# Optimization experiments

Measured on AMD Instinct MI355X. Metric: run time of the kernel, lower is better.

Reference implementation:

```python
import jax, jax.numpy as jnp
import numpy as np
import math

K = 8       # wavelet order (k)
C = 8       # channels (c)
ALPHA = 64  # retained Fourier modes
L = 0       # coarsest level
B = 32
N = 8192    # power of two


def setup_inputs() -> dict:
    key = jax.random.key(0)
    ks = jax.random.split(key, 14)
    ck = C * K
    scale = 1.0 / (ck * ck)  # matches torch: 1/(c*k)**2
    f32 = jnp.float32
    inp = {
        "x": jax.random.normal(ks[0], (B, N, C, K), dtype=f32),
        # SparseKernelFT1d weights (complex, stored as re/im): scale * rand
        "wA_re": scale * jax.random.uniform(ks[1], (ck, ck, ALPHA), dtype=f32),
        "wA_im": scale * jax.random.uniform(ks[2], (ck, ck, ALPHA), dtype=f32),
        "wB_re": scale * jax.random.uniform(ks[3], (ck, ck, ALPHA), dtype=f32),
        "wB_im": scale * jax.random.uniform(ks[4], (ck, ck, ALPHA), dtype=f32),
        "wC_re": scale * jax.random.uniform(ks[5], (ck, ck, ALPHA), dtype=f32),
        "wC_im": scale * jax.random.uniform(ks[6], (ck, ck, ALPHA), dtype=f32),
        # T0 linear layer (k -> k)
        "T0_w": jax.random.normal(ks[7], (K, K), dtype=f32) / math.sqrt(K),
        "T0_b": 0.01 * jax.random.normal(ks[8], (K,), dtype=f32),
        # Legendre wavelet filter buffers: ec_* are [H0.T;H1.T] / [G0.T;G1.T] (2k,k),
        # rc_* are [H0;G0] / [H1;G1] (2k,k). Stand-ins: random orthonormal-ish matrices
        # scaled like wavelet filters (same math regardless of exact values).
        "ec_s": jax.random.normal(ks[9], (2 * K, K), dtype=f32) / math.sqrt(2 * K),
        "ec_d": jax.random.normal(ks[10], (2 * K, K), dtype=f32) / math.sqrt(2 * K),
        "rc_e": jax.random.normal(ks[11], (2 * K, K), dtype=f32) / math.sqrt(2 * K),
        "rc_o": jax.random.normal(ks[12], (2 * K, K), dtype=f32) / math.sqrt(2 * K),
    }
    return inp


def _sparse_ft(x, w_re, w_im):
    # x: [B, N, c, k] -> spectral mixing over first ALPHA rfft modes
    Bb, Nn, c, k = x.shape
    xv = x.reshape(Bb, Nn, c * k).transpose(0, 2, 1)   # [B, ck, N]
    xf = jnp.fft.rfft(xv)                               # [B, ck, N//2+1] complex
    l = min(ALPHA, Nn // 2 + 1)
    W = (w_re[:, :, :l] + 1j * w_im[:, :, :l]).astype(jnp.complex64)
    of = jnp.einsum('bix,iox->box', xf[:, :, :l], W)
    out_ft = jnp.zeros((Bb, c * k, Nn // 2 + 1), dtype=jnp.complex64).at[:, :, :l].set(of)
    xo = jnp.fft.irfft(out_ft, n=Nn)                    # [B, ck, N] real
    return xo.transpose(0, 2, 1).reshape(Bb, Nn, c, k)


def reference(x, wA_re, wA_im, wB_re, wB_im, wC_re, wC_im, T0_w, T0_b,
              ec_s, ec_d, rc_e, rc_o):
    Bb, Nn, c, k = x.shape
    ns = int(math.floor(math.log2(Nn)))
    Ud, Us = [], []
    # --- decomposition ---
    for _ in range(ns - L):
        xa = jnp.concatenate([x[:, ::2], x[:, 1::2]], axis=-1)  # [B, N/2, c, 2k]
        d = xa @ ec_d                                           # [B, N/2, c, k]
        s = xa @ ec_s
        Ud.append(_sparse_ft(d, wA_re, wA_im) + _sparse_ft(s, wB_re, wB_im))
        Us.append(_sparse_ft(d, wC_re, wC_im))
        x = s
    # --- coarsest-level linear ---
    x = x @ T0_w.T + T0_b
    # --- reconstruction (u_s is None branch) ---
    for i in range(ns - 1 - L, -1, -1):
        x = x + Us[i]
        xc = jnp.concatenate([x, Ud[i]], axis=-1)               # [B, n, c, 2k]
        x_e = xc @ rc_e
        x_o = xc @ rc_o
        Bc, Nc, cc, _ = xc.shape
        x = jnp.stack([x_e, x_o], axis=2).reshape(Bc, Nc * 2, cc, K)  # interleave even/odd
    return (x,) + tuple(Ud) + tuple(Us)
```

## Files before the change

kernel.cpp:

```cpp
#include <hip/hip_runtime.h>

#define BB 32
#define CKD 64
#define CC 8
#define KK 8
#define FPW 132

__device__ const int D_FCB[14] = {0,32,48,56,60,62,63,64,65,66,67,68,69,70};
__device__ const int D_TB[14] = {0,64,96,112,120,124,126,127,128,129,130,131,132,133};
__device__ const int D_L[13]  = {64,64,64,64,64,64,33,17,9,5,3,2,1};
__device__ const int D_FTOF[13] = {0,524288,786432,917504,983040,1015808,1032192,
                                   1048576,1064960,1081344,1097728,1114112,1130496};
__device__ const int D_XP[65] = {0,13,25,36,46,56,65,74,83,92,100,108,116,124,132,140,
    148,156,163,170,177,184,191,198,205,212,219,226,233,240,247,254,261,268,274,280,
    286,292,298,304,310,316,322,328,334,340,346,352,358,364,370,376,382,388,394,400,
    406,412,418,424,430,436,442,448,454};

typedef __attribute__((ext_vector_type(4))) short s4v;
typedef __attribute__((ext_vector_type(8))) short s8v;
typedef __attribute__((ext_vector_type(4))) float f4v;

static __device__ __forceinline__ float4 ld4(const float* p){ return *(const float4*)p; }
static __device__ __forceinline__ size_t d_udo(int i){ return 33554432ull - (16777216u >> i); }
static __device__ __forceinline__ size_t d_uso(int i){ return 50329600ull - (16777216u >> i); }
static __device__ __forceinline__ size_t d_tof(int i){ return 128ull * (8192u - (8192u >> i)); }

static __device__ __forceinline__ unsigned short b16(float f) {
    unsigned u = __float_as_uint(f);
    u += 0x7FFFu + ((u >> 16) & 1u);
    return (unsigned short)(u >> 16);
}
static __device__ __forceinline__ float fb16(unsigned short h) {
    return __uint_as_float(((unsigned)h) << 16);
}

__global__ __launch_bounds__(256) void gen_tbl2_k(unsigned short* __restrict__ Th,
        unsigned short* __restrict__ Tl, unsigned short* __restrict__ Tfh,
        unsigned short* __restrict__ Tfl) {
    int lvl = blockIdx.y;
    int nh = 4096 >> lvl;
    int idx = blockIdx.x * 256 + threadIdx.x;
    if (blockIdx.z == 0) {
        if (idx >= nh * 128) return;
        int t = idx >> 7, k = idx & 127, x = k >> 1;
        int l = nh / 2 + 1; if (l > 64) l = 64;
        float v = 0.f;
        if (x < l) {
            int r = (x * t) & (nh - 1);
            float th = 6.283185307179586f * ((float)r / (float)nh);
            float s, c; sincosf(th, &s, &c);
            v = (k & 1) ? s : c;
        }
        unsigned short hi = b16(v);
        unsigned short lo = b16(v - fb16(hi));
        size_t off = d_tof(lvl) + idx;
        Th[off] = hi; Tl[off] = lo;
    } else {
        int nhp = nh < 128 ? 128 : nh;
        if (idx >= 128 * nhp) return;
        int j = idx & 7;
        int lane = (idx >> 3) & 63;
        int mt = (idx >> 9) & 7;
        int kb = idx >> 12;
        int row = mt*16 + (lane & 15);
        int t = kb*32 + (lane >> 4)*8 + j;
        int x = row >> 1;
        int l = nh / 2 + 1; if (l > 64) l = 64;
        float v = 0.f;
        if (x < l && t < nh) {
            int r = (x * t) & (nh - 1);
            float th = 6.283185307179586f * ((float)r / (float)nh);
            float s, c; sincosf(th, &s, &c);
            v = (row & 1) ? -s : c;
        }
        unsigned short hi = b16(v);
        unsigned short lo = b16(v - fb16(hi));
        size_t off = (size_t)D_FTOF[lvl] + idx;
        Tfh[off] = hi; Tfl[off] = lo;
    }
}

__global__ __launch_bounds__(256) void wtr_k(const float* __restrict__ wAr,
        const float* __restrict__ wAi, const float* __restrict__ wBr,
        const float* __restrict__ wBi, const float* __restrict__ wCr,
        const float* __restrict__ wCi, float* __restrict__ wt) {
    int x = blockIdx.x, arr = blockIdx.y;
    const float* W;
    switch (arr) {
        case 0: W = wAr; break;
        case 1: W = wAi; break;
        case 2: W = wBr; break;
        case 3: W = wBi; break;
        case 4: W = wCr; break;
        default: W = wCi; break;
    }
    float* o = wt + ((size_t)arr*64 + x)*4096;
    for (int q = threadIdx.x; q < 4096; q += 256)
        o[q] = W[(size_t)q*64 + x];
}

__global__ __launch_bounds__(256) void wbig_k(const float* __restrict__ wt,
        unsigned short* __restrict__ wbh, unsigned short* __restrict__ wbl) {
    int x = blockIdx.x;
    int f0 = blockIdx.y * 2048;
    for (int q = threadIdx.x; q < 2048; q += 256) {
        int f = f0 + q;
        int j = f & 7;
        int lane = (f >> 3) & 63;
        int nt = (f >> 9) & 15;
        int kt = f >> 13;
        int k = kt*32 + (lane >> 4)*8 + j;
        int n = nt*16 + (lane & 15);
        int pk = k >> 6, i = k & 63;
        int pn = n >> 6, o = n & 63;
        int arr; float sgn;
        switch ((pn << 2) | pk) {
            case 0:  arr = 0; sgn =  1.f; break;
            case 1:  arr = 1; sgn = -1.f; break;
            case 2:  arr = 2; sgn =  1.f; break;
            case 3:  arr = 3; sgn = -1.f; break;
            case 4:  arr = 1; sgn = -1.f; break;
            case 5:  arr = 0; sgn = -1.f; break;
            case 6:  arr = 3; sgn = -1.f; break;
            case 7:  arr = 2; sgn = -1.f; break;
            case 8:  arr = 4; sgn =  1.f; break;
            case 9:  arr = 5; sgn = -1.f; break;
            case 12: arr = 5; sgn = -1.f; break;
            case 13: arr = 4; sgn = -1.f; break;
            default: arr = -1; sgn = 0.f; break;
        }
        float v = 0.f;
        if (arr >= 0) v = sgn * wt[((size_t)arr*64 + x)*4096 + (size_t)i*64 + o];
        unsigned short h = b16(v);
        unsigned short l2 = b16(v - fb16(h));
        wbh[(size_t)x*65536 + f] = h;
        wbl[(size_t)x*65536 + f] = l2;
    }
}

__global__ __launch_bounds__(256) void decomp_k(const float* __restrict__ xin,
        const float* __restrict__ ecd, const float* __restrict__ ecs,
        float* __restrict__ dslot, float* __restrict__ sslot, int nh) {
    int idx = blockIdx.x * 256 + threadIdx.x;
    if (idx >= BB * nh * CC) return;
    int c = idx & 7;
    int t = (idx >> 3) % nh;
    int b = idx / (nh * CC);
    const float* p0 = xin + ((size_t)b * 2 * nh + 2 * t) * CKD + c * KK;
    float xa[16];
    float4 v;
    v = ld4(p0);      xa[0]=v.x; xa[1]=v.y; xa[2]=v.z; xa[3]=v.w;
    v = ld4(p0+4);    xa[4]=v.x; xa[5]=v.y; xa[6]=v.z; xa[7]=v.w;
    v = ld4(p0+64);   xa[8]=v.x; xa[9]=v.y; xa[10]=v.z; xa[11]=v.w;
    v = ld4(p0+68);   xa[12]=v.x; xa[13]=v.y; xa[14]=v.z; xa[15]=v.w;
    float dd[8], ss[8];
    #pragma unroll
    for (int m = 0; m < 8; m++) { dd[m] = 0.f; ss[m] = 0.f; }
    #pragma unroll
    for (int j = 0; j < 16; j++) {
        float xv = xa[j];
        #pragma unroll
        for (int m = 0; m < 8; m++) {
            dd[m] = fmaf(xv, ecd[j*8+m], dd[m]);
            ss[m] = fmaf(xv, ecs[j*8+m], ss[m]);
        }
    }
    size_t ob = ((size_t)b * nh + t) * CKD + c * KK;
    *(float4*)(dslot+ob)   = make_float4(dd[0],dd[1],dd[2],dd[3]);
    *(float4*)(dslot+ob+4) = make_float4(dd[4],dd[5],dd[6],dd[7]);
    *(float4*)(sslot+ob)   = make_float4(ss[0],ss[1],ss[2],ss[3]);
    *(float4*)(sslot+ob+4) = make_float4(ss[4],ss[5],ss[6],ss[7]);
}

__global__ __launch_bounds__(256) void decomp_small_k(const float* __restrict__ s4base,
        const float* __restrict__ ecd, const float* __restrict__ ecs,
        const float* __restrict__ T0w, const float* __restrict__ T0b,
        float* __restrict__ outbuf, float* __restrict__ xt0) {
    __shared__ float sA[128*64];
    __shared__ float sB[64*64];
    int b = blockIdx.x, tid = threadIdx.x;
    for (int lvl = 5; lvl <= 12; lvl++) {
        int nh = 4096 >> lvl;
        const float* src = (lvl == 5) ? (s4base + (size_t)b*256*CKD)
                                      : (((lvl - 6) & 1) ? sB : sA);
        float* dst = ((lvl - 5) & 1) ? sB : sA;
        float* dG = outbuf + d_udo(lvl) + (size_t)b*nh*CKD;
        float* sG = outbuf + d_uso(lvl) + (size_t)b*nh*CKD;
        for (int q = tid; q < nh*8; q += 256) {
            int c = q & 7, t = q >> 3;
            const float* p0 = src + (size_t)(2*t)*CKD + c*KK;
            float xa[16];
            float4 v;
            v = ld4(p0);      xa[0]=v.x; xa[1]=v.y; xa[2]=v.z; xa[3]=v.w;
            v = ld4(p0+4);    xa[4]=v.x; xa[5]=v.y; xa[6]=v.z; xa[7]=v.w;
            v = ld4(p0+64);   xa[8]=v.x; xa[9]=v.y; xa[10]=v.z; xa[11]=v.w;
            v = ld4(p0+68);   xa[12]=v.x; xa[13]=v.y; xa[14]=v.z; xa[15]=v.w;
            float dd[8], ss[8];
            #pragma unroll
            for (int m = 0; m < 8; m++) { dd[m] = 0.f; ss[m] = 0.f; }
            #pragma unroll
            for (int j = 0; j < 16; j++) {
                float xv = xa[j];
                #pragma unroll
                for (int m = 0; m < 8; m++) {
                    dd[m] = fmaf(xv, ecd[j*8+m], dd[m]);
                    ss[m] = fmaf(xv, ecs[j*8+m], ss[m]);
                }
            }
            size_t ob = (size_t)t * CKD + c * KK;
            *(float4*)(dG+ob)   = make_float4(dd[0],dd[1],dd[2],dd[3]);
            *(float4*)(dG+ob+4) = make_float4(dd[4],dd[5],dd[6],dd[7]);
            *(float4*)(sG+ob)   = make_float4(ss[0],ss[1],ss[2],ss[3]);
            *(float4*)(sG+ob+4) = make_float4(ss[4],ss[5],ss[6],ss[7]);
            float* dl = dst + t*CKD + c*KK;
            #pragma unroll
            for (int j = 0; j < 8; j++) dl[j] = ss[j];
        }
        __syncthreads();
    }
    if (tid < 64) {
        int m = tid & 7, c = tid >> 3;
        const float* xr = sB + c*KK;
        float a = T0b[m];
        #pragma unroll
        for (int j = 0; j < 8; j++) a = fmaf(xr[j], T0w[m*8+j], a);
        xt0[(size_t)b*64 + tid] = a;
    }
}

__global__ __launch_bounds__(256) void fft_fwd_mfma_k(const float* __restrict__ outbuf,
        const unsigned short* __restrict__ Tfh, const unsigned short* __restrict__ Tfl,
        float* __restrict__ xfpf, float2* __restrict__ xf_all) {
    __shared__ unsigned vp[128*FPW];
    int slot = blockIdx.x;
    int lvl = 0;
    while (lvl < 12 && slot >= D_FCB[lvl+1]) lvl++;
    int nh = 4096 >> lvl;
    int ch = D_FCB[lvl+1] - D_FCB[lvl];
    int t0s = (slot - D_FCB[lvl]) * 128;
    int b = blockIdx.y;
    const float* V0 = outbuf + d_udo(lvl) + (size_t)b * nh * CKD;
    const float* V1 = outbuf + d_uso(lvl) + (size_t)b * nh * CKD;
    const unsigned short* THb = Tfh + D_FTOF[lvl];
    const unsigned short* TLb = Tfl + D_FTOF[lvl];
    int tid = threadIdx.x;
    int w = tid >> 6, lane = tid & 63;
    int col = lane & 15, khi = lane >> 4;
    int mt0 = w * 2;
    #pragma unroll
    for (int q = 0; q < 16; q++) {
        int fi = tid + 256*q;
        int tl_ = fi >> 5;
        int t = t0s + tl_;
        int iq = fi & 31;
        int z = iq >> 4;
        int i4 = (iq & 15) * 4;
        const float* Vz = z ? V1 : V0;
        float4 v = make_float4(0.f,0.f,0.f,0.f);
        if (t < nh) v = ld4(Vz + (size_t)t*CKD + i4);
        const float* pv = &v.x;
        int rowb = z*64 + i4;
        #pragma unroll
        for (int j = 0; j < 4; j++) {
            int row = rowb + j;
            float f = pv[j];
            unsigned u = __float_as_uint(f);
            unsigned hi = u & 0xFFFF0000u;
            float r = f - __uint_as_float(hi);
            unsigned lo = __float_as_uint(r) & 0xFFFF0000u;
            int cw = tl_ ^ (((row >> 3) & 7) << 2);
            vp[row*FPW + cw] = (hi >> 16) | lo;
        }
    }
    __syncthreads();
    int rrow[8], rswz[8];
    #pragma unroll
    for (int n = 0; n < 8; n++) {
        rrow[n] = n*16 + col;
        rswz[n] = ((rrow[n] >> 3) & 7) << 2;
    }
    f4v acc[2][8];
    #pragma unroll
    for (int m = 0; m < 2; m++)
        #pragma unroll
        for (int n = 0; n < 8; n++) acc[m][n] = (f4v){0.f,0.f,0.f,0.f};
    int kb0 = (slot - D_FCB[lvl]) * 4;
    #pragma unroll
    for (int kk = 0; kk < 4; kk++) {
        int kb = kb0 + kk;
        s8v ah[2], al[2];
        #pragma unroll
        for (int m = 0; m < 2; m++) {
            size_t fo = (((size_t)kb*8 + (mt0 + m))*64 + lane)*8;
            ah[m] = *(const s8v*)(THb + fo);
            al[m] = *(const s8v*)(TLb + fo);
        }
        int cb = kk*32 + khi*8;
        #pragma unroll
        for (int n = 0; n < 8; n++) {
            const unsigned* pr = vp + rrow[n]*FPW;
            uint4 w0 = *(const uint4*)(pr + (cb ^ rswz[n]));
            uint4 w1 = *(const uint4*)(pr + ((cb + 4) ^ rswz[n]));
            s8v bh, bl;
            const unsigned* pw = &w0.x;
            #pragma unroll
            for (int j = 0; j < 4; j++) {
                bh[j] = (short)(pw[j] & 0xFFFFu);
                bl[j] = (short)(pw[j] >> 16);
            }
            pw = &w1.x;
            #pragma unroll
            for (int j = 0; j < 4; j++) {
                bh[4+j] = (short)(pw[j] & 0xFFFFu);
                bl[4+j] = (short)(pw[j] >> 16);
            }
            #pragma unroll
            for (int m = 0; m < 2; m++) {
                acc[m][n] = __builtin_amdgcn_mfma_f32_16x16x32_bf16(ah[m], bh, acc[m][n], 0,0,0);
                acc[m][n] = __builtin_amdgcn_mfma_f32_16x16x32_bf16(ah[m], bl, acc[m][n], 0,0,0);
                acc[m][n] = __builtin_amdgcn_mfma_f32_16x16x32_bf16(al[m], bh, acc[m][n], 0,0,0);
            }
        }
    }
    if (ch == 1) {
        float* XB = (float*)xf_all + (size_t)lvl*524288 + (size_t)b*16384;
        #pragma unroll
        for (int m = 0; m < 2; m++) {
            int m0 = (mt0 + m)*16 + khi*4;
            #pragma unroll
            for (int n = 0; n < 8; n++) {
                int ic = n*16 + col;
                int z = ic >> 6, i = ic & 63;
                float* X = XB + (size_t)z*8192;
                #pragma unroll
                for (int r = 0; r < 4; r++) {
                    int row = m0 + r;
                    X[(((size_t)(row >> 1)*64 + i) << 1) | (row & 1)] = acc[m][n][r];
                }
            }
        }
    } else {
        #pragma unroll
        for (int m = 0; m < 2; m++) {
            int m0 = (mt0 + m)*16 + khi*4;
            #pragma unroll
            for (int n = 0; n < 8; n++) {
                int ic = n*16 + col;
                int z = ic >> 6, i = ic & 63;
                float* P = xfpf + ((size_t)slot*64 + (size_t)b*2 + z) * 8192;
                #pragma unroll
                for (int r = 0; r < 4; r++)
                    P[(size_t)(m0 + r)*64 + i] = acc[m][n][r];
            }
        }
    }
}

__global__ __launch_bounds__(256) void reduce_fwd_k(const float* __restrict__ xfpf,
        float2* __restrict__ xf_all) {
    int lvl = blockIdx.y;
    int e = blockIdx.x * 256 + threadIdx.x;
    int j = e & 4095;
    int bz = e >> 12;
    int x = j >> 6, i = j & 63;
    int c0 = D_FCB[lvl], c1 = D_FCB[lvl+1];
    float re = 0.f, im = 0.f;
    for (int c = c0; c < c1; c++) {
        size_t base = ((size_t)c*64 + bz) * 8192;
        re += xfpf[base + (size_t)(2*x)*64 + i];
        im += xfpf[base + (size_t)(2*x+1)*64 + i];
    }
    xf_all[(size_t)lvl*262144 + (size_t)bz*4096 + j] = make_float2(re, im);
}

__global__ __launch_bounds__(256) void mix_mfma_k(const float2* __restrict__ xf_all,
        const unsigned short* __restrict__ wbh, const unsigned short* __restrict__ wbl,
        unsigned short* __restrict__ ofh, unsigned short* __restrict__ ofl) {
    __shared__ unsigned ax[32*260];
    int x = 0;
    while (x < 64 && (int)blockIdx.x >= D_XP[x+1]) x++;
    int lvl = blockIdx.x - D_XP[x];
    int nh = 4096 >> lvl;
    const float2* xfL = xf_all + (size_t)lvl*262144;
    int tid = threadIdx.x;
    for (int q = tid; q < 4096; q += 256) {
        int b = q >> 7, z = (q >> 6) & 1, i = q & 63;
        float2 v = xfL[((size_t)b*2 + z)*4096 + (size_t)x*64 + i];
        int sw = ((b >> 3) & 7) << 2;
        int kR = z*128 + i;
        unsigned uR = __float_as_uint(v.x);
        unsigned hiR = uR & 0xFFFF0000u;
        float rR = v.x - __uint_as_float(hiR);
        unsigned loR = __float_as_uint(rR) & 0xFFFF0000u;
        ax[b*260 + (kR ^ sw)] = (hiR >> 16) | loR;
        unsigned uI = __float_as_uint(v.y);
        unsigned hiI = uI & 0xFFFF0000u;
        float rI = v.y - __uint_as_float(hiI);
        unsigned loI = __float_as_uint(rI) & 0xFFFF0000u;
        ax[b*260 + ((kR + 64) ^ sw)] = (hiI >> 16) | loI;
    }
    __syncthreads();
    int w4 = tid >> 6, lane = tid & 63;
    int col = lane & 15, khi = lane >> 4;
    int mt = w4 & 1, nt0 = (w4 >> 1) * 8;
    int arow = mt*16 + col;
    int asw = ((arow >> 3) & 7) << 2;
    const unsigned* ap = ax + arow*260;
    const unsigned short* WBH = wbh + (size_t)x*65536;
    const unsigned short* WBL = wbl + (size_t)x*65536;
    f4v acc[8];
    #pragma unroll
    for (int n = 0; n < 8; n++) acc[n] = (f4v){0.f,0.f,0.f,0.f};
    #pragma unroll
    for (int kt = 0; kt < 8; kt++) {
        int cb = kt*32 + khi*8;
        uint4 a0 = *(const uint4*)(ap + (cb ^ asw));
        uint4 a1 = *(const uint4*)(ap + ((cb + 4) ^ asw));
        s8v ah, al;
        const unsigned* pw = &a0.x;
        #pragma unroll
        for (int j = 0; j < 4; j++) {
            ah[j] = (short)(pw[j] & 0xFFFFu);
            al[j] = (short)(pw[j] >> 16);
        }
        pw = &a1.x;
        #pragma unroll
        for (int j = 0; j < 4; j++) {
            ah[4+j] = (short)(pw[j] & 0xFFFFu);
            al[4+j] = (short)(pw[j] >> 16);
        }
        #pragma unroll
        for (int n = 0; n < 8; n++) {
            int nt = nt0 + n;
            size_t fo = (((size_t)kt*16 + nt)*64 + lane)*8;
            s8v bh = *(const s8v*)(WBH + fo);
            s8v bl = *(const s8v*)(WBL + fo);
            acc[n] = __builtin_amdgcn_mfma_f32_16x16x32_bf16(ah, bh, acc[n], 0, 0, 0);
            acc[n] = __builtin_amdgcn_mfma_f32_16x16x32_bf16(ah, bl, acc[n], 0, 0, 0);
            acc[n] = __builtin_amdgcn_mfma_f32_16x16x32_bf16(al, bh, acc[n], 0, 0, 0);
        }
    }
    float wfac = (x == 0 || 2*x == nh) ? 1.f : 2.f;
    float sc = wfac / (float)nh;
    int k0 = 2*x;
    #pragma unroll
    for (int n = 0; n < 8; n++) {
        int nn = nt0 + n;
        int pn = nn >> 2;
        int o = (nn & 3)*16 + col;
        int z = pn >> 1;
        int kr = k0 + (pn & 1);
        #pragma unroll
        for (int r = 0; r < 4; r++) {
            int b = mt*16 + khi*4 + r;
            size_t base = (((size_t)lvl*32 + b)*2 + z)*8192 + (size_t)kr*64 + o;
            float v = sc * acc[n][r];
            unsigned short h = b16(v);
            unsigned short l2 = b16(v - fb16(h));
            ofh[base] = h;
            ofl[base] = l2;
        }
    }
}

__global__ __launch_bounds__(256) void fft_inv_mfma_k(
        const unsigned short* __restrict__ ofh, const unsigned short* __restrict__ ofl,
        const unsigned short* __restrict__ Th,  const unsigned short* __restrict__ Tl,
        float* __restrict__ outbuf) {
    __shared__ unsigned short gh[2*64*132];
    __shared__ unsigned short gl[2*64*132];
    int lvl = 0;
    while (lvl < 12 && (int)blockIdx.x >= D_TB[lvl+1]) lvl++;
    int g = blockIdx.x - D_TB[lvl];
    int nh = 4096 >> lvl;
    int tbase = g * 64;
    int b = blockIdx.y;
    int tid = threadIdx.x;
    #pragma unroll
    for (int q = 0; q < 8; q++) {
        int fi = tid + 256*q;
        int z = fi >> 10;
        int r = fi & 1023;
        int k = r & 127, oct = r >> 7;
        const unsigned short* Gh = ofh + (((size_t)lvl*32 + b)*2 + z)*8192;
        const unsigned short* Gl = ofl + (((size_t)lvl*32 + b)*2 + z)*8192;
        uint4 vh = *(const uint4*)(Gh + (size_t)k*64 + oct*8);
        uint4 vl = *(const uint4*)(Gl + (size_t)k*64 + oct*8);
        const unsigned* ph = &vh.x;
        const unsigned* pl = &vl.x;
        #pragma unroll
        for (int i = 0; i < 8; i++) {
            unsigned wd = ph[i>>1];
            gh[z*8448 + (oct*8+i)*132 + k] = (i&1) ? (unsigned short)(wd>>16) : (unsigned short)(wd&0xFFFF);
            wd = pl[i>>1];
            gl[z*8448 + (oct*8+i)*132 + k] = (i&1) ? (unsigned short)(wd>>16) : (unsigned short)(wd&0xFFFF);
        }
    }
    __syncthreads();
    int w = tid >> 6;
    int lane = tid & 63;
    int tb = tbase + w*16;
    if (tb >= nh) return;
    int trow = lane & 15, khi = lane >> 4;
    int tA = tb + trow; if (tA >= nh) tA = nh - 1;
    const unsigned short* THp = Th + d_tof(lvl) + (size_t)tA*128 + khi*8;
    const unsigned short* TLp = Tl + d_tof(lvl) + (size_t)tA*128 + khi*8;
    f4v acc[8];
    #pragma unroll
    for (int n = 0; n < 8; n++) acc[n] = (f4v){0.f,0.f,0.f,0.f};
    #pragma unroll
    for (int kk = 0; kk < 4; kk++) {
        s8v ah = *(const s8v*)(THp + kk*32);
        s8v al = *(const s8v*)(TLp + kk*32);
        #pragma unroll
        for (int n = 0; n < 8; n++) {
            int z = n >> 2;
            int off = z*8448 + ((n & 3)*16 + trow)*132 + kk*32 + khi*8;
            s4v b0 = *(const s4v*)(gh + off);
            s4v b1 = *(const s4v*)(gh + off + 4);
            s4v c0 = *(const s4v*)(gl + off);
            s4v c1 = *(const s4v*)(gl + off + 4);
            s8v bh = __builtin_shufflevector(b0, b1, 0,1,2,3,4,5,6,7);
            s8v bl = __builtin_shufflevector(c0, c1, 0,1,2,3,4,5,6,7);
            acc[n] = __builtin_amdgcn_mfma_f32_16x16x32_bf16(ah, bh, acc[n], 0, 0, 0);
            acc[n] = __builtin_amdgcn_mfma_f32_16x16x32_bf16(ah, bl, acc[n], 0, 0, 0);
            acc[n] = __builtin_amdgcn_mfma_f32_16x16x32_bf16(al, bh, acc[n], 0, 0, 0);
        }
    }
    float* U0 = outbuf + d_udo(lvl) + (size_t)b * nh * CKD;
    float* U1 = outbuf + d_uso(lvl) + (size_t)b * nh * CKD;
    int thi4 = khi * 4;
    #pragma unroll
    for (int n = 0; n < 8; n++) {
        float* U = (n >> 2) ? U1 : U0;
        int ocol = (n & 3)*16 + trow;
        #pragma unroll
        for (int r = 0; r < 4; r++) {
            int t = tb + thi4 + r;
            if (t < nh) U[(size_t)t*64 + ocol] = acc[n][r];
        }
    }
}

__global__ __launch_bounds__(256) void recon_small_k(const float* __restrict__ xt0,
        const float* __restrict__ outbuf,
        const float* __restrict__ rce, const float* __restrict__ rco,
        float* __restrict__ rb0) {
    __shared__ float xA[128*64];
    __shared__ float xB[64*64];
    int b = blockIdx.x, tid = threadIdx.x;
    if (tid < 64) xB[tid] = xt0[(size_t)b*64 + tid];
    __syncthreads();
    for (int i = 12; i >= 6; i--) {
        int nh = 4096 >> i;
        const float* cur = ((i == 12) || !(i & 1)) ? xB : xA;
        float* nxt = (i & 1) ? xB : xA;
        const float* Us = outbuf + d_uso(i) + (size_t)b*nh*CKD;
        const float* Ud = outbuf + d_udo(i) + (size_t)b*nh*CKD;
        for (int q = tid; q < nh*8; q += 256) {
            int c = q & 7, t = q >> 3;
            size_t base = (size_t)t*CKD + c*KK;
            float xc[16];
            float4 a0 = ld4(cur+base), a1 = ld4(cur+base+4);
            float4 u0 = ld4(Us+base),  u1 = ld4(Us+base+4);
            float4 d0 = ld4(Ud+base),  d1 = ld4(Ud+base+4);
            xc[0]=a0.x+u0.x; xc[1]=a0.y+u0.y; xc[2]=a0.z+u0.z; xc[3]=a0.w+u0.w;
            xc[4]=a1.x+u1.x; xc[5]=a1.y+u1.y; xc[6]=a1.z+u1.z; xc[7]=a1.w+u1.w;
            xc[8]=d0.x;  xc[9]=d0.y;  xc[10]=d0.z; xc[11]=d0.w;
            xc[12]=d1.x; xc[13]=d1.y; xc[14]=d1.z; xc[15]=d1.w;
            float e[8], o2[8];
            #pragma unroll
            for (int m = 0; m < 8; m++) { e[m] = 0.f; o2[m] = 0.f; }
            #pragma unroll
            for (int j = 0; j < 16; j++) {
                float xv = xc[j];
                #pragma unroll
                for (int m = 0; m < 8; m++) {
                    e[m]  = fmaf(xv, rce[j*8+m], e[m]);
                    o2[m] = fmaf(xv, rco[j*8+m], o2[m]);
                }
            }
            if (i > 6) {
                float* pe = nxt + (size_t)(2*t)*CKD + c*KK;
                #pragma unroll
                for (int j = 0; j < 8; j++) { pe[j] = e[j]; pe[CKD + j] = o2[j]; }
            } else {
                float* pe = rb0 + ((size_t)b*128 + 2*t)*CKD + c*KK;
                *(float4*)(pe)      = make_float4(e[0],e[1],e[2],e[3]);
                *(float4*)(pe+4)    = make_float4(e[4],e[5],e[6],e[7]);
                *(float4*)(pe+64)   = make_float4(o2[0],o2[1],o2[2],o2[3]);
                *(float4*)(pe+68)   = make_float4(o2[4],o2[5],o2[6],o2[7]);
            }
        }
        __syncthreads();
    }
}

__global__ __launch_bounds__(256) void recon_k(const float* __restrict__ xin,
        const float* __restrict__ us, const float* __restrict__ ud,
        const float* __restrict__ rce, const float* __restrict__ rco,
        float* __restrict__ xout, int nh) {
    int idx = blockIdx.x*256 + threadIdx.x;
    if (idx >= BB*nh*CC) return;
    int c = idx & 7;
    int t = (idx >> 3) % nh;
    int b = idx / (nh*CC);
    size_t base = ((size_t)b*nh + t)*CKD + c*KK;
    float xc[16];
    float4 a0 = ld4(xin+base), a1 = ld4(xin+base+4);
    float4 u0 = ld4(us+base),  u1 = ld4(us+base+4);
    float4 d0 = ld4(ud+base),  d1 = ld4(ud+base+4);
    xc[0]=a0.x+u0.x; xc[1]=a0.y+u0.y; xc[2]=a0.z+u0.z; xc[3]=a0.w+u0.w;
    xc[4]=a1.x+u1.x; xc[5]=a1.y+u1.y; xc[6]=a1.z+u1.z; xc[7]=a1.w+u1.w;
    xc[8]=d0.x;  xc[9]=d0.y;  xc[10]=d0.z; xc[11]=d0.w;
    xc[12]=d1.x; xc[13]=d1.y; xc[14]=d1.z; xc[15]=d1.w;
    float e[8], o2[8];
    #pragma unroll
    for (int m = 0; m < 8; m++) { e[m] = 0.f; o2[m] = 0.f; }
    #pragma unroll
    for (int j = 0; j < 16; j++) {
        float xv = xc[j];
        #pragma unroll
        for (int m = 0; m < 8; m++) {
            e[m]  = fmaf(xv, rce[j*8+m], e[m]);
            o2[m] = fmaf(xv, rco[j*8+m], o2[m]);
        }
    }
    size_t ob = ((size_t)b*2*nh + 2*t)*CKD + c*KK;
    *(float4*)(xout+ob)      = make_float4(e[0],e[1],e[2],e[3]);
    *(float4*)(xout+ob+4)    = make_float4(e[4],e[5],e[6],e[7]);
    *(float4*)(xout+ob+64)   = make_float4(o2[0],o2[1],o2[2],o2[3]);
    *(float4*)(xout+ob+68)   = make_float4(o2[4],o2[5],o2[6],o2[7]);
}

extern "C" void kernel_launch(void* const* d_in, const int* in_sizes, int n_in,
                              void* d_out, int out_size, void* d_ws, size_t ws_size,
                              hipStream_t stream) {
    const float* x   = (const float*)d_in[0];
    const float* wAr = (const float*)d_in[1];
    const float* wAi = (const float*)d_in[2];
    const float* wBr = (const float*)d_in[3];
    const float* wBi = (const float*)d_in[4];
    const float* wCr = (const float*)d_in[5];
    const float* wCi = (const float*)d_in[6];
    const float* T0w = (const float*)d_in[7];
    const float* T0b = (const float*)d_in[8];
    const float* ecs = (const float*)d_in[9];
    const float* ecd = (const float*)d_in[10];
    const float* rce = (const float*)d_in[11];
    const float* rco = (const float*)d_in[12];
    float* out = (float*)d_out;
    float* wsf = (float*)d_ws;

    size_t p = 0;
    float2* xf_all = (float2*)(wsf + p); p += 6815744;
    unsigned short* ofh = (unsigned short*)(wsf + p); p += 3407872;
    unsigned short* ofl = (unsigned short*)(wsf + p); p += 3407872;
    unsigned short* Th  = (unsigned short*)(wsf + p); p += 528384;
    unsigned short* Tl  = (unsigned short*)(wsf + p); p += 528384;
    unsigned short* Tfh = (unsigned short*)(wsf + p); p += 573440;
    unsigned short* Tfl = (unsigned short*)(wsf + p); p += 573440;
    float*  wt   = wsf + p; p += 1572864;
    unsigned short* wbh = (unsigned short*)(wsf + p); p += 2097152;
    unsigned short* wbl = (unsigned short*)(wsf + p); p += 2097152;
    float*  xt0  = wsf + p; p += 2048;
    float*  rb0  = wsf + p; p += 4194304;
    float*  rb1  = wsf + p; p += 8388608;
    float*  xfpf = wsf + p; p += 36700160;
    (void)ws_size; (void)in_sizes; (void)n_in; (void)out_size;

    size_t udo[13], uso[13];
    for (int i = 0; i < 13; i++) {
        udo[i] = 33554432ull - (16777216u >> i);
        uso[i] = 50329600ull - (16777216u >> i);
    }

    gen_tbl2_k<<<dim3(2048, 13, 2), 256, 0, stream>>>(Th, Tl, Tfh, Tfl);
    wtr_k<<<dim3(64, 6), 256, 0, stream>>>(wAr, wAi, wBr, wBi, wCr, wCi, wt);
    wbig_k<<<dim3(64, 32), 256, 0, stream>>>(wt, wbh, wbl);

    for (int i = 0; i < 5; i++) {
        int nh = 4096 >> i;
        const float* xin_l = (i == 0) ? x : (out + uso[i-1]);
        int tot = BB * nh * CC;
        decomp_k<<<(tot + 255)/256, 256, 0, stream>>>(xin_l, ecd, ecs, out + udo[i], out + uso[i], nh);
    }
    decomp_small_k<<<BB, 256, 0, stream>>>(out + uso[4], ecd, ecs, T0w, T0b, out, xt0);

    fft_fwd_mfma_k<<<dim3(70, BB), 256, 0, stream>>>(out, Tfh, Tfl, xfpf, xf_all);
    reduce_fwd_k<<<dim3(1024, 5), 256, 0, stream>>>(xfpf, xf_all);
    mix_mfma_k<<<454, 256, 0, stream>>>(xf_all, wbh, wbl, ofh, ofl);
    fft_inv_mfma_k<<<dim3(133, BB), 256, 0, stream>>>(ofh, ofl, Th, Tl, out);

    recon_small_k<<<BB, 256, 0, stream>>>(xt0, out, rce, rco, rb0);
    const float* rin = rb0;
    for (int i = 5; i >= 0; i--) {
        int nh = 4096 >> i;
        float* ro = (i == 0) ? out : ((i & 1) ? rb1 : rb0);
        int tot = BB * nh * CC;
        recon_k<<<(tot + 255)/256, 256, 0, stream>>>(rin, out + uso[i], out + udo[i], rce, rco, ro, nh);
        rin = ro;
    }
}
```

Baseline: 434.4 us.

## Loop forward-DFT blocks over multiple chunks and pack hi/lo spectrum words

Each forward-DFT block now loops over up to four 128-row chunks and accumulates in registers. This cuts the block count and the number of partial sums that go to the reduction kernel, which now only covers three levels. Separately, the mixed spectrum is stored as one packed 32-bit word holding the bf16 hi and lo halves instead of two separate arrays, and the inverse-DFT kernel loads and unpacks it. The risk is less parallelism in the forward kernel (768 blocks instead of 2240), plus extra syncthreads per chunk.

```diff
diff --git a/kernel.cpp b/kernel.cpp
--- a/kernel.cpp
+++ b/kernel.cpp
@@ -6,7 +6,7 @@
 #define KK 8
 #define FPW 132
 
-__device__ const int D_FCB[14] = {0,32,48,56,60,62,63,64,65,66,67,68,69,70};
+__device__ const int D_FCB[14] = {0,8,12,14,15,16,17,18,19,20,21,22,23,24};
 __device__ const int D_TB[14] = {0,64,96,112,120,124,126,127,128,129,130,131,132,133};
 __device__ const int D_L[13]  = {64,64,64,64,64,64,33,17,9,5,3,2,1};
 __device__ const int D_FTOF[13] = {0,524288,786432,917504,983040,1015808,1032192,
@@ -236,8 +236,10 @@
     int lvl = 0;
     while (lvl < 12 && slot >= D_FCB[lvl+1]) lvl++;
     int nh = 4096 >> lvl;
-    int ch = D_FCB[lvl+1] - D_FCB[lvl];
-    int t0s = (slot - D_FCB[lvl]) * 128;
+    int nslots = D_FCB[lvl+1] - D_FCB[lvl];
+    int tiles = nh >= 128 ? (nh >> 7) : 1;
+    int cs = (slot - D_FCB[lvl]) * 4;
+    int ce = cs + 4; if (ce > tiles) ce = tiles;
     int b = blockIdx.y;
     const float* V0 = outbuf + d_udo(lvl) + (size_t)b * nh * CKD;
     const float* V1 = outbuf + d_uso(lvl) + (size_t)b * nh * CKD;
@@ -247,32 +249,6 @@
     int w = tid >> 6, lane = tid & 63;
     int col = lane & 15, khi = lane >> 4;
     int mt0 = w * 2;
-    #pragma unroll
-    for (int q = 0; q < 16; q++) {
-        int fi = tid + 256*q;
-        int tl_ = fi >> 5;
-        int t = t0s + tl_;
-        int iq = fi & 31;
-        int z = iq >> 4;
-        int i4 = (iq & 15) * 4;
-        const float* Vz = z ? V1 : V0;
-        float4 v = make_float4(0.f,0.f,0.f,0.f);
-        if (t < nh) v = ld4(Vz + (size_t)t*CKD + i4);
-        const float* pv = &v.x;
-        int rowb = z*64 + i4;
-        #pragma unroll
-        for (int j = 0; j < 4; j++) {
-            int row = rowb + j;
-            float f = pv[j];
-            unsigned u = __float_as_uint(f);
-            unsigned hi = u & 0xFFFF0000u;
-            float r = f - __uint_as_float(hi);
-            unsigned lo = __float_as_uint(r) & 0xFFFF0000u;
-            int cw = tl_ ^ (((row >> 3) & 7) << 2);
-            vp[row*FPW + cw] = (hi >> 16) | lo;
-        }
-    }
-    __syncthreads();
     int rrow[8], rswz[8];
     #pragma unroll
     for (int n = 0; n < 8; n++) {
@@ -284,45 +260,74 @@
     for (int m = 0; m < 2; m++)
         #pragma unroll
         for (int n = 0; n < 8; n++) acc[m][n] = (f4v){0.f,0.f,0.f,0.f};
-    int kb0 = (slot - D_FCB[lvl]) * 4;
-    #pragma unroll
-    for (int kk = 0; kk < 4; kk++) {
-        int kb = kb0 + kk;
-        s8v ah[2], al[2];
-        #pragma unroll
-        for (int m = 0; m < 2; m++) {
-            size_t fo = (((size_t)kb*8 + (mt0 + m))*64 + lane)*8;
-            ah[m] = *(const s8v*)(THb + fo);
-            al[m] = *(const s8v*)(TLb + fo);
-        }
-        int cb = kk*32 + khi*8;
-        #pragma unroll
-        for (int n = 0; n < 8; n++) {
-            const unsigned* pr = vp + rrow[n]*FPW;
-            uint4 w0 = *(const uint4*)(pr + (cb ^ rswz[n]));
-            uint4 w1 = *(const uint4*)(pr + ((cb + 4) ^ rswz[n]));
-            s8v bh, bl;
-            const unsigned* pw = &w0.x;
+    for (int c = cs; c < ce; c++) {
+        int t0s = c * 128;
+        __syncthreads();
+        #pragma unroll
+        for (int q = 0; q < 16; q++) {
+            int fi = tid + 256*q;
+            int tl_ = fi >> 5;
+            int t = t0s + tl_;
+            int iq = fi & 31;
+            int z = iq >> 4;
+            int i4 = (iq & 15) * 4;
+            const float* Vz = z ? V1 : V0;
+            float4 v = make_float4(0.f,0.f,0.f,0.f);
+            if (t < nh) v = ld4(Vz + (size_t)t*CKD + i4);
+            const float* pv = &v.x;
+            int rowb = z*64 + i4;
             #pragma unroll
             for (int j = 0; j < 4; j++) {
-                bh[j] = (short)(pw[j] & 0xFFFFu);
-                bl[j] = (short)(pw[j] >> 16);
-            }
-            pw = &w1.x;
-            #pragma unroll
-            for (int j = 0; j < 4; j++) {
-                bh[4+j] = (short)(pw[j] & 0xFFFFu);
-                bl[4+j] = (short)(pw[j] >> 16);
-            }
+                int row = rowb + j;
+                float f = pv[j];
+                unsigned u = __float_as_uint(f);
+                unsigned hi = u & 0xFFFF0000u;
+                float r = f - __uint_as_float(hi);
+                unsigned lo = __float_as_uint(r) & 0xFFFF0000u;
+                int cw = tl_ ^ (((row >> 3) & 7) << 2);
+                vp[row*FPW + cw] = (hi >> 16) | lo;
+            }
+        }
+        __syncthreads();
+        #pragma unroll
+        for (int kk = 0; kk < 4; kk++) {
+            int kb = c*4 + kk;
+            s8v ah[2], al[2];
             #pragma unroll
             for (int m = 0; m < 2; m++) {
-                acc[m][n] = __builtin_amdgcn_mfma_f32_16x16x32_bf16(ah[m], bh, acc[m][n], 0,0,0);
-                acc[m][n] = __builtin_amdgcn_mfma_f32_16x16x32_bf16(ah[m], bl, acc[m][n], 0,0,0);
-                acc[m][n] = __builtin_amdgcn_mfma_f32_16x16x32_bf16(al[m], bh, acc[m][n], 0,0,0);
-            }
-        }
-    }
-    if (ch == 1) {
+                size_t fo = (((size_t)kb*8 + (mt0 + m))*64 + lane)*8;
+                ah[m] = *(const s8v*)(THb + fo);
+                al[m] = *(const s8v*)(TLb + fo);
+            }
+            int cb = kk*32 + khi*8;
+            #pragma unroll
+            for (int n = 0; n < 8; n++) {
+                const unsigned* pr = vp + rrow[n]*FPW;
+                uint4 w0 = *(const uint4*)(pr + (cb ^ rswz[n]));
+                uint4 w1 = *(const uint4*)(pr + ((cb + 4) ^ rswz[n]));
+                s8v bh, bl;
+                const unsigned* pw = &w0.x;
+                #pragma unroll
+                for (int j = 0; j < 4; j++) {
+                    bh[j] = (short)(pw[j] & 0xFFFFu);
+                    bl[j] = (short)(pw[j] >> 16);
+                }
+                pw = &w1.x;
+                #pragma unroll
+                for (int j = 0; j < 4; j++) {
+                    bh[4+j] = (short)(pw[j] & 0xFFFFu);
+                    bl[4+j] = (short)(pw[j] >> 16);
+                }
+                #pragma unroll
+                for (int m = 0; m < 2; m++) {
+                    acc[m][n] = __builtin_amdgcn_mfma_f32_16x16x32_bf16(ah[m], bh, acc[m][n], 0,0,0);
+                    acc[m][n] = __builtin_amdgcn_mfma_f32_16x16x32_bf16(ah[m], bl, acc[m][n], 0,0,0);
+                    acc[m][n] = __builtin_amdgcn_mfma_f32_16x16x32_bf16(al[m], bh, acc[m][n], 0,0,0);
+                }
+            }
+        }
+    }
+    if (nslots == 1) {
         float* XB = (float*)xf_all + (size_t)lvl*524288 + (size_t)b*16384;
         #pragma unroll
         for (int m = 0; m < 2; m++) {
@@ -375,7 +380,7 @@
 
 __global__ __launch_bounds__(256) void mix_mfma_k(const float2* __restrict__ xf_all,
         const unsigned short* __restrict__ wbh, const unsigned short* __restrict__ wbl,
-        unsigned short* __restrict__ ofh, unsigned short* __restrict__ ofl) {
+        unsigned* __restrict__ ofp) {
     __shared__ unsigned ax[32*260];
     int x = 0;
     while (x < 64 && (int)blockIdx.x >= D_XP[x+1]) x++;
@@ -457,18 +462,16 @@
             float v = sc * acc[n][r];
             unsigned short h = b16(v);
             unsigned short l2 = b16(v - fb16(h));
-            ofh[base] = h;
-            ofl[base] = l2;
+            ofp[base] = (unsigned)h | ((unsigned)l2 << 16);
         }
     }
 }
 
 __global__ __launch_bounds__(256) void fft_inv_mfma_k(
-        const unsigned short* __restrict__ ofh, const unsigned short* __restrict__ ofl,
+        const unsigned* __restrict__ ofp,
         const unsigned short* __restrict__ Th,  const unsigned short* __restrict__ Tl,
         float* __restrict__ outbuf) {
-    __shared__ unsigned short gh[2*64*132];
-    __shared__ unsigned short gl[2*64*132];
+    __shared__ unsigned gp[2*64*132];
     int lvl = 0;
     while (lvl < 12 && (int)blockIdx.x >= D_TB[lvl+1]) lvl++;
     int g = blockIdx.x - D_TB[lvl];
@@ -476,25 +479,18 @@
     int tbase = g * 64;
     int b = blockIdx.y;
     int tid = threadIdx.x;
-    #pragma unroll
-    for (int q = 0; q < 8; q++) {
+    const unsigned* Gp = ofp + (((size_t)lvl*32 + b)*2)*8192;
+    #pragma unroll
+    for (int q = 0; q < 16; q++) {
         int fi = tid + 256*q;
-        int z = fi >> 10;
-        int r = fi & 1023;
-        int k = r & 127, oct = r >> 7;
-        const unsigned short* Gh = ofh + (((size_t)lvl*32 + b)*2 + z)*8192;
-        const unsigned short* Gl = ofl + (((size_t)lvl*32 + b)*2 + z)*8192;
-        uint4 vh = *(const uint4*)(Gh + (size_t)k*64 + oct*8);
-        uint4 vl = *(const uint4*)(Gl + (size_t)k*64 + oct*8);
-        const unsigned* ph = &vh.x;
-        const unsigned* pl = &vl.x;
-        #pragma unroll
-        for (int i = 0; i < 8; i++) {
-            unsigned wd = ph[i>>1];
-            gh[z*8448 + (oct*8+i)*132 + k] = (i&1) ? (unsigned short)(wd>>16) : (unsigned short)(wd&0xFFFF);
-            wd = pl[i>>1];
-            gl[z*8448 + (oct*8+i)*132 + k] = (i&1) ? (unsigned short)(wd>>16) : (unsigned short)(wd&0xFFFF);
-        }
+        int z = fi >> 11;
+        int rem = fi & 2047;
+        int k = rem >> 4, o4 = (rem & 15)*4;
+        uint4 v = *(const uint4*)(Gp + (size_t)z*8192 + (size_t)k*64 + o4);
+        const unsigned* pw = &v.x;
+        #pragma unroll
+        for (int i = 0; i < 4; i++)
+            gp[z*8448 + (o4+i)*132 + k] = pw[i];
     }
     __syncthreads();
     int w = tid >> 6;
@@ -516,12 +512,21 @@
         for (int n = 0; n < 8; n++) {
             int z = n >> 2;
             int off = z*8448 + ((n & 3)*16 + trow)*132 + kk*32 + khi*8;
-            s4v b0 = *(const s4v*)(gh + off);
-            s4v b1 = *(const s4v*)(gh + off + 4);
-            s4v c0 = *(const s4v*)(gl + off);
-            s4v c1 = *(const s4v*)(gl + off + 4);
-            s8v bh = __builtin_shufflevector(b0, b1, 0,1,2,3,4,5,6,7);
-            s8v bl = __builtin_shufflevector(c0, c1, 0,1,2,3,4,5,6,7);
+            uint4 w0 = *(const uint4*)(gp + off);
+            uint4 w1 = *(const uint4*)(gp + off + 4);
+            s8v bh, bl;
+            const unsigned* pw = &w0.x;
+            #pragma unroll
+            for (int j = 0; j < 4; j++) {
+                bh[j] = (short)(pw[j] & 0xFFFFu);
+                bl[j] = (short)(pw[j] >> 16);
+            }
+            pw = &w1.x;
+            #pragma unroll
+            for (int j = 0; j < 4; j++) {
+                bh[4+j] = (short)(pw[j] & 0xFFFFu);
+                bl[4+j] = (short)(pw[j] >> 16);
+            }
             acc[n] = __builtin_amdgcn_mfma_f32_16x16x32_bf16(ah, bh, acc[n], 0, 0, 0);
             acc[n] = __builtin_amdgcn_mfma_f32_16x16x32_bf16(ah, bl, acc[n], 0, 0, 0);
             acc[n] = __builtin_amdgcn_mfma_f32_16x16x32_bf16(al, bh, acc[n], 0, 0, 0);
@@ -654,8 +659,7 @@
 
     size_t p = 0;
     float2* xf_all = (float2*)(wsf + p); p += 6815744;
-    unsigned short* ofh = (unsigned short*)(wsf + p); p += 3407872;
-    unsigned short* ofl = (unsigned short*)(wsf + p); p += 3407872;
+    unsigned* ofp = (unsigned*)(wsf + p); p += 6815744;
     unsigned short* Th  = (unsigned short*)(wsf + p); p += 528384;
     unsigned short* Tl  = (unsigned short*)(wsf + p); p += 528384;
     unsigned short* Tfh = (unsigned short*)(wsf + p); p += 573440;
@@ -687,10 +691,10 @@
     }
     decomp_small_k<<<BB, 256, 0, stream>>>(out + uso[4], ecd, ecs, T0w, T0b, out, xt0);
 
-    fft_fwd_mfma_k<<<dim3(70, BB), 256, 0, stream>>>(out, Tfh, Tfl, xfpf, xf_all);
-    reduce_fwd_k<<<dim3(1024, 5), 256, 0, stream>>>(xfpf, xf_all);
-    mix_mfma_k<<<454, 256, 0, stream>>>(xf_all, wbh, wbl, ofh, ofl);
-    fft_inv_mfma_k<<<dim3(133, BB), 256, 0, stream>>>(ofh, ofl, Th, Tl, out);
+    fft_fwd_mfma_k<<<dim3(24, BB), 256, 0, stream>>>(out, Tfh, Tfl, xfpf, xf_all);
+    reduce_fwd_k<<<dim3(1024, 3), 256, 0, stream>>>(xfpf, xf_all);
+    mix_mfma_k<<<454, 256, 0, stream>>>(xf_all, wbh, wbl, ofp);
+    fft_inv_mfma_k<<<dim3(133, BB), 256, 0, stream>>>(ofp, Th, Tl, out);
 
     recon_small_k<<<BB, 256, 0, stream>>>(xt0, out, rce, rco, rb0);
     const float* rin = rb0;
```

Result: no change. 438.2 us (+0.9%).
